# Performance work log

Measured on AMD Instinct MI355X. Metric: run time of the kernel, lower is better.

## Reference

```python
import jax, jax.numpy as jnp
import numpy as np

H = 2048          # hidden_size
I_MOE = 1408      # moe_intermediate_size (per expert)
I_SH = 5632       # shared_expert_intermediate_size
E = 8             # num_experts
TOP_K = 2         # num_experts_per_tok
B, S = 1, 2048


def setup_inputs() -> dict:
    key = jax.random.key(0)
    ks = jax.random.split(key, 7)
    sc = 0.02
    return {
        "hidden_states": jax.random.normal(ks[0], (B, S, H), jnp.float32),
        "W_router": jax.random.normal(ks[1], (E, H), jnp.float32) * sc,      # gate.weight
        "W_sgate": jax.random.normal(ks[2], (1, H), jnp.float32) * sc,       # shared_expert_gate.weight
        "Ws_gate_up": jax.random.normal(ks[3], (H, 2 * I_SH), jnp.float32) * sc,  # shared expert merged gate/up
        "Ws_down": jax.random.normal(ks[4], (I_SH, H), jnp.float32) * sc,
        "We_gate_up": jax.random.normal(ks[5], (E, H, 2 * I_MOE), jnp.float32) * sc,  # stacked expert gate/up
        "We_down": jax.random.normal(ks[6], (E, I_MOE, H), jnp.float32) * sc,
    }


def _silu_and_mul(gu, inter):
    # gate_up layout: [..., 2*inter] -> silu(gate) * up, matching SiluAndMul
    return jax.nn.silu(gu[..., :inter]) * gu[..., inter:]


def reference(hidden_states, W_router, W_sgate, Ws_gate_up, Ws_down, We_gate_up, We_down):
    orig_shape = hidden_states.shape
    x = hidden_states.reshape(-1, H)                     # [T, H]
    T = x.shape[0]

    # --- router: softmax in fp32 then top-k (NOT renormalized, as in source) ---
    logits = x @ W_router.T                              # [T, E]
    probs = jax.nn.softmax(logits.astype(jnp.float32), axis=-1)
    rw, sel = jax.lax.top_k(probs, TOP_K)                # [T, K]
    rw = rw.astype(x.dtype)

    # sparse combine matrix [T, E]: routing weight where selected, else 0
    combine = jnp.zeros((T, E), x.dtype).at[jnp.arange(T)[:, None], sel].add(rw)

    # --- shared expert ---
    sh = _silu_and_mul(x @ Ws_gate_up, I_SH) @ Ws_down    # [T, H]
    shared_out = sh * jax.nn.sigmoid(x @ W_sgate.T)       # [T, H]

    # --- experts: dense dispatch (math-identical to gather/MLP/index_add loop) ---
    gu = jnp.einsum('th,ehi->eti', x, We_gate_up)         # [E, T, 2*I_MOE]
    h = _silu_and_mul(gu, I_MOE)                          # [E, T, I_MOE]
    eo = jnp.einsum('eti,eih->eth', h, We_down)           # [E, T, H]
    sparse_out = jnp.einsum('eth,te->th', eo, combine)    # [T, H]

    return (shared_out + sparse_out).reshape(orig_shape)
```

## Files before the change

kernel.cpp:

```cpp
#include <hip/hip_runtime.h>
#include <cstdio>


#define H_DIM 2048
#define IMOE  1408
#define ISH   5632
#define NEXP  8
#define T_TOK 2048
#define TK_TOT (T_TOK * 2)

typedef __attribute__((ext_vector_type(8))) short short8;
typedef __attribute__((ext_vector_type(8))) __bf16 bf16x8;
typedef __attribute__((ext_vector_type(4))) float f32x4;

__device__ __forceinline__ float bf2f(unsigned short u) {
  union { unsigned int i; float f; } v; v.i = ((unsigned int)u) << 16; return v.f;
}
__device__ __forceinline__ unsigned short f2bf(float f) {
  union { float f; unsigned int i; } v; v.f = f;
  unsigned int x = v.i;
  return (unsigned short)((x + 0x7fffu + ((x >> 16) & 1u)) >> 16);
}

__device__ __forceinline__ f32x4 MFMA16(short8 a, short8 b, f32x4 c) {
  return __builtin_amdgcn_mfma_f32_16x16x32_bf16(
      __builtin_bit_cast(bf16x8, a), __builtin_bit_cast(bf16x8, b), c, 0, 0, 0);
}

__device__ __forceinline__ void gload_lds16(const unsigned short* g, unsigned short* l) {
  __builtin_amdgcn_global_load_lds(
      (const __attribute__((address_space(1))) unsigned int*)g,
      (__attribute__((address_space(3))) unsigned int*)l, 16, 0, 0);
}

__device__ __forceinline__ float silu_f(float x) { return x / (1.0f + __expf(-x)); }

#define SBAR()   asm volatile("s_barrier" ::: "memory")
#define VMCNT(n) asm volatile("s_waitcnt vmcnt(" #n ")" ::: "memory")


__global__ __launch_bounds__(256)
void transpose_cvt_kernel(const float* __restrict__ src, unsigned short* __restrict__ dst,
                          int R, int C, long sStride, long dStride) {
  src += (long)blockIdx.z * sStride;
  dst += (long)blockIdx.z * dStride;
  __shared__ float tile[32][33];
  int tx = threadIdx.x, ty = threadIdx.y;
  int x = blockIdx.x * 32 + tx;
  int yb = blockIdx.y * 32;
#pragma unroll
  for (int j = 0; j < 4; j++) {
    int y = yb + ty + j * 8;
    tile[ty + j * 8][tx] = src[(long)y * C + x];
  }
  __syncthreads();
  int c = blockIdx.x * 32 + ty;
  int r = yb + tx;
#pragma unroll
  for (int j = 0; j < 4; j++) {
    dst[(long)(c + j * 8) * R + r] = f2bf(tile[tx][ty + j * 8]);
  }
}

__global__ __launch_bounds__(256)
void cvt_x_kernel(const float* __restrict__ x, unsigned short* __restrict__ xb, int total4) {
  int i = blockIdx.x * 256 + threadIdx.x;
  if (i >= total4) return;
  float4 v = ((const float4*)x)[i];
  ushort4 o;
  o.x = f2bf(v.x); o.y = f2bf(v.y); o.z = f2bf(v.z); o.w = f2bf(v.w);
  ((ushort4*)xb)[i] = o;
}


__global__ __launch_bounds__(256)
void router_kernel(const float* __restrict__ x, const float* __restrict__ Wr,
                   const float* __restrict__ Wsg, float* __restrict__ rw,
                   int* __restrict__ sel, float* __restrict__ sgate_sig,
                   int* __restrict__ counts) {
  int t = blockIdx.x;
  const float* xr = x + (long)t * H_DIM;
  float p[9];
#pragma unroll
  for (int e = 0; e < 9; e++) p[e] = 0.0f;
  for (int h = threadIdx.x; h < H_DIM; h += 256) {
    float xv = xr[h];
#pragma unroll
    for (int e = 0; e < 8; e++) p[e] += xv * Wr[e * H_DIM + h];
    p[8] += xv * Wsg[h];
  }
#pragma unroll
  for (int e = 0; e < 9; e++)
    for (int off = 32; off > 0; off >>= 1)
      p[e] += __shfl_down(p[e], off, 64);
  __shared__ float red[4][9];
  int wave = threadIdx.x >> 6, lane = threadIdx.x & 63;
  if (lane == 0) {
#pragma unroll
    for (int e = 0; e < 9; e++) red[wave][e] = p[e];
  }
  __syncthreads();
  if (threadIdx.x == 0) {
    float lg[9];
#pragma unroll
    for (int e = 0; e < 9; e++) lg[e] = red[0][e] + red[1][e] + red[2][e] + red[3][e];
    float m = lg[0];
#pragma unroll
    for (int e = 1; e < 8; e++) m = fmaxf(m, lg[e]);
    float pr[8], s = 0.0f;
#pragma unroll
    for (int e = 0; e < 8; e++) { pr[e] = expf(lg[e] - m); s += pr[e]; }
    float inv = 1.0f / s;
#pragma unroll
    for (int e = 0; e < 8; e++) pr[e] *= inv;
    int i0 = 0;
#pragma unroll
    for (int e = 1; e < 8; e++) if (pr[e] > pr[i0]) i0 = e;
    int i1 = (i0 == 0) ? 1 : 0;
#pragma unroll
    for (int e = 0; e < 8; e++) if (e != i0 && pr[e] > pr[i1]) i1 = e;
    rw[t * 2] = pr[i0]; rw[t * 2 + 1] = pr[i1];
    sel[t * 2] = i0;    sel[t * 2 + 1] = i1;
    sgate_sig[t] = 1.0f / (1.0f + expf(-lg[8]));
    atomicAdd(&counts[i0], 1);
    atomicAdd(&counts[i1], 1);
  }
}

__global__ void scan_kernel(const int* __restrict__ counts, int* __restrict__ offsets) {
  if (threadIdx.x == 0 && blockIdx.x == 0) {
    int s = 0;
    for (int e = 0; e < NEXP; e++) { offsets[e] = s; s += counts[e]; }
    offsets[NEXP] = s;
  }
}

__global__ __launch_bounds__(256)
void scatter_kernel(const int* __restrict__ sel, const int* __restrict__ offsets,
                    int* __restrict__ cursor, int* __restrict__ tok_of_slot,
                    int* __restrict__ slot_of_tok) {
  int t = blockIdx.x * 256 + threadIdx.x;
  if (t >= T_TOK) return;
#pragma unroll
  for (int k = 0; k < 2; k++) {
    int e = sel[t * 2 + k];
    int pos = atomicAdd(&cursor[e], 1);
    int slot = offsets[e] + pos;
    tok_of_slot[slot] = t;
    slot_of_tok[t * 2 + k] = slot;
  }
}

template <int EPI, bool EXPERT, bool GATHER>
__global__ __launch_bounds__(512, 2)
void gemm8_kernel(const unsigned short* __restrict__ A,
                  const unsigned short* __restrict__ BT,
                  void* __restrict__ Cv,
                  int N, int Kld, int KLEN, int M,
                  const int* __restrict__ counts, const int* __restrict__ offsets,
                  const int* __restrict__ tok_of_slot,
                  const float* __restrict__ rowscale, long bt_estride) {
  __shared__ unsigned short lds8[65536];

  int cnt = M, rowbase = 0, k0 = 0;
  const unsigned short* bt = BT;
  if constexpr (EXPERT) {
    int e = blockIdx.z;
    cnt = counts[e];
    rowbase = offsets[e];
    bt += (long)e * bt_estride;
  } else {
    k0 = blockIdx.z * KLEN;
  }
  int row0 = blockIdx.x * 256;
  if (row0 >= cnt) return;
  int col0 = blockIdx.y * 256;

  int tid = threadIdx.x, wave = tid >> 6, lane = tid & 63;
  int NT = KLEN / 32;

  const unsigned short* aSrc[2];
  const unsigned short* bSrc[2];
#pragma unroll
  for (int i = 0; i < 2; i++) {
    int r = i * 128 + (tid >> 2);
    int sw = (((tid & 3) ^ ((r >> 1) & 3)) * 8);
    long arow;
    if constexpr (EXPERT) {
      int s = rowbase + min(row0 + r, cnt - 1);
      arow = GATHER ? tok_of_slot[s] : s;
    } else {
      arow = row0 + r;
    }
    aSrc[i] = A + arow * (long)Kld + k0 + sw;
    bSrc[i] = bt + (long)(col0 + r) * Kld + k0 + sw;
  }
  int dA0 = wave * 512, dA1 = 4096 + wave * 512;
  int dB0 = 8192 + wave * 512, dB1 = 12288 + wave * 512;

  auto STAGE_A = [&](int u) {
    int b2 = (u & 3) * 16384;
    long kk = (long)min(u, NT - 1) * 32;
    gload_lds16(aSrc[0] + kk, &lds8[b2 + dA0]);
    gload_lds16(aSrc[1] + kk, &lds8[b2 + dA1]);
  };
  auto STAGE_B = [&](int u) {
    int b2 = (u & 3) * 16384;
    long kk = (long)min(u, NT - 1) * 32;
    gload_lds16(bSrc[0] + kk, &lds8[b2 + dB0]);
    gload_lds16(bSrc[1] + kk, &lds8[b2 + dB1]);
  };

  int wr = wave >> 2, wc = wave & 3;
  int fr = lane & 15, fg = lane >> 4;
  int addrA0[4], addrA1[4], addrB[4];
#pragma unroll
  for (int m = 0; m < 4; m++) {
    int rl0 = wr * 128 + m * 16 + fr;
    int rl1 = rl0 + 64;
    int cl  = wc * 64 + m * 16 + fr;
    addrA0[m] = rl0 * 32 + ((fg ^ ((rl0 >> 1) & 3)) * 8);
    addrA1[m] = rl1 * 32 + ((fg ^ ((rl1 >> 1) & 3)) * 8);
    addrB[m]  = 8192 + cl * 32 + ((fg ^ ((cl >> 1) & 3)) * 8);
  }

  STAGE_A(0); STAGE_B(0);
  STAGE_A(1); STAGE_B(1);
  STAGE_A(2); STAGE_B(2);
  VMCNT(8);
  SBAR();

  f32x4 acc[8][4] = {};

  for (int t = 0; t < NT; t++) {
    int b = (t & 3) * 16384;
    int u = t + 3;
    short8 Bf[4], Af[4];
#pragma unroll
    for (int n = 0; n < 4; n++) Bf[n] = *(const short8*)&lds8[b + addrB[n]];
#pragma unroll
    for (int m = 0; m < 4; m++) Af[m] = *(const short8*)&lds8[b + addrA0[m]];
    STAGE_A(u);
    SBAR();
    __builtin_amdgcn_s_setprio(1);
#pragma unroll
    for (int m = 0; m < 4; m++)
#pragma unroll
      for (int n = 0; n < 4; n++)
        acc[m][n] = MFMA16(Af[m], Bf[n], acc[m][n]);
    __builtin_amdgcn_s_setprio(0);
    SBAR();
#pragma unroll
    for (int m = 0; m < 4; m++) Af[m] = *(const short8*)&lds8[b + addrA1[m]];
    STAGE_B(u);
    SBAR();
    __builtin_amdgcn_s_setprio(1);
#pragma unroll
    for (int m = 0; m < 4; m++)
#pragma unroll
      for (int n = 0; n < 4; n++)
        acc[4 + m][n] = MFMA16(Af[m], Bf[n], acc[4 + m][n]);
    __builtin_amdgcn_s_setprio(0);
    VMCNT(8);
    SBAR();
  }
  VMCNT(0);

  int rowguard = cnt - row0;
#pragma unroll
  for (int mq = 0; mq < 8; mq++) {
    int rl = wr * 128 + (mq >> 2) * 64 + (mq & 3) * 16 + fg * 4;
#pragma unroll
    for (int n = 0; n < 4; n++) {
      int cg = col0 + wc * 64 + n * 16 + fr;
      f32x4 v = acc[mq][n];
#pragma unroll
      for (int j = 0; j < 4; j++) {
        int r = rl + j;
        if (r < rowguard) {
          long orow = (long)rowbase + row0 + r;
          long ci = orow * (long)N + cg;
          if constexpr (EPI == 0)      ((unsigned short*)Cv)[ci] = f2bf(v[j]);
          else if constexpr (EPI == 2) ((float*)Cv)[ci] = v[j];
          else unsafeAtomicAdd(&((float*)Cv)[ci], v[j] * rowscale[orow]);
        }
      }
    }
  }
}


__global__ __launch_bounds__(256)
void silu_mul_kernel(const unsigned short* __restrict__ gu, unsigned short* __restrict__ h,
                     int rows, int I) {
  int i = blockIdx.x * 256 + threadIdx.x;
  int i4 = I >> 2;
  if (i >= rows * i4) return;
  int row = i / i4;
  int ci = (i - row * i4) * 4;
  const unsigned short* g = gu + (long)row * 2 * I + ci;
  ushort4 gv = *(const ushort4*)g;
  ushort4 uv = *(const ushort4*)(g + I);
  ushort4 o;
  o.x = f2bf(silu_f(bf2f(gv.x)) * bf2f(uv.x));
  o.y = f2bf(silu_f(bf2f(gv.y)) * bf2f(uv.y));
  o.z = f2bf(silu_f(bf2f(gv.z)) * bf2f(uv.z));
  o.w = f2bf(silu_f(bf2f(gv.w)) * bf2f(uv.w));
  *(ushort4*)(h + (long)row * I + ci) = o;
}

__global__ __launch_bounds__(256)
void combine_kernel(float* __restrict__ out, const float* __restrict__ eo,
                    const int* __restrict__ slot_of_tok, const float* __restrict__ rw) {
  int i = blockIdx.x * 256 + threadIdx.x;
  const int h4n = H_DIM / 4;
  if (i >= T_TOK * h4n) return;
  int t = i / h4n;
  int h4 = i - t * h4n;
  int s0 = slot_of_tok[t * 2], s1 = slot_of_tok[t * 2 + 1];
  float w0 = rw[t * 2], w1 = rw[t * 2 + 1];
  float4 o = ((float4*)out)[i];
  float4 a = ((const float4*)eo)[(long)s0 * h4n + h4];
  float4 b = ((const float4*)eo)[(long)s1 * h4n + h4];
  o.x += w0 * a.x + w1 * b.x;
  o.y += w0 * a.y + w1 * b.y;
  o.z += w0 * a.z + w1 * b.z;
  o.w += w0 * a.w + w1 * b.w;
  ((float4*)out)[i] = o;
}


extern "C" void kernel_launch(void* const* d_in, const int* in_sizes, int n_in,
                              void* d_out, int out_size, void* d_ws, size_t ws_size,
                              hipStream_t stream) {
  (void)in_sizes; (void)n_in; (void)out_size;
  const float* x    = (const float*)d_in[0];
  const float* Wr   = (const float*)d_in[1];
  const float* Wsg  = (const float*)d_in[2];
  const float* Wsgu = (const float*)d_in[3];
  const float* Wsd  = (const float*)d_in[4];
  const float* Wegu = (const float*)d_in[5];
  const float* Wed  = (const float*)d_in[6];
  float* out = (float*)d_out;

  char* ws = (char*)d_ws;
  size_t off = 0;
  auto alloc = [&](size_t b) { size_t o = off; off += (b + 255) & ~(size_t)255; return o; };

  size_t o_xbf   = alloc((size_t)T_TOK * H_DIM * 2);
  size_t o_WsguT = alloc((size_t)2 * ISH * H_DIM * 2);
  size_t o_WsdT  = alloc((size_t)H_DIM * ISH * 2);
  size_t o_WeguT = alloc((size_t)NEXP * 2 * IMOE * H_DIM * 2);
  size_t o_WedT  = alloc((size_t)NEXP * H_DIM * IMOE * 2);
  size_t o_gush  = alloc((size_t)T_TOK * 2 * ISH * 2);
  size_t o_hsh   = alloc((size_t)T_TOK * ISH * 2);
  size_t o_ints  = alloc(256);
  size_t o_rw    = alloc((size_t)TK_TOT * 4);
  size_t o_sel   = alloc((size_t)TK_TOT * 4);
  size_t o_sg    = alloc((size_t)T_TOK * 4);
  size_t o_tok   = alloc((size_t)TK_TOT * 4);
  size_t o_s2t   = alloc((size_t)TK_TOT * 4);

  if (off > ws_size) {
    fprintf(stderr, "[moe kernel] workspace too small: need %zu have %zu\n", off, ws_size);
    return;
  }

  unsigned short* xbf   = (unsigned short*)(ws + o_xbf);
  unsigned short* WsguT = (unsigned short*)(ws + o_WsguT);
  unsigned short* WsdT  = (unsigned short*)(ws + o_WsdT);
  unsigned short* WeguT = (unsigned short*)(ws + o_WeguT);
  unsigned short* WedT  = (unsigned short*)(ws + o_WedT);
  unsigned short* gu_sh = (unsigned short*)(ws + o_gush);
  unsigned short* h_sh  = (unsigned short*)(ws + o_hsh);
  unsigned short* gu_e = (unsigned short*)(ws + o_gush);
  unsigned short* h_e  = (unsigned short*)(ws + o_gush + (size_t)TK_TOT * 2 * IMOE * 2);
  float* eo = (float*)(ws + o_WsguT);

  int* counts  = (int*)(ws + o_ints);
  int* cursor  = counts + 8;
  int* offsets = counts + 16;
  float* rw    = (float*)(ws + o_rw);
  int* sel     = (int*)(ws + o_sel);
  float* sgate = (float*)(ws + o_sg);
  int* tok     = (int*)(ws + o_tok);
  int* s2t     = (int*)(ws + o_s2t);

  dim3 tb(32, 8, 1);

  hipMemsetAsync(counts, 0, 64, stream);

  transpose_cvt_kernel<<<dim3(2 * ISH / 32, H_DIM / 32, 1), tb, 0, stream>>>(
      Wsgu, WsguT, H_DIM, 2 * ISH, 0, 0);
  transpose_cvt_kernel<<<dim3(H_DIM / 32, ISH / 32, 1), tb, 0, stream>>>(
      Wsd, WsdT, ISH, H_DIM, 0, 0);
  transpose_cvt_kernel<<<dim3(2 * IMOE / 32, H_DIM / 32, NEXP), tb, 0, stream>>>(
      Wegu, WeguT, H_DIM, 2 * IMOE, (long)H_DIM * 2 * IMOE, (long)2 * IMOE * H_DIM);
  transpose_cvt_kernel<<<dim3(H_DIM / 32, IMOE / 32, NEXP), tb, 0, stream>>>(
      Wed, WedT, IMOE, H_DIM, (long)IMOE * H_DIM, (long)H_DIM * IMOE);

  cvt_x_kernel<<<(T_TOK * H_DIM / 4) / 256, 256, 0, stream>>>(x, xbf, T_TOK * H_DIM / 4);

  router_kernel<<<T_TOK, 256, 0, stream>>>(x, Wr, Wsg, rw, sel, sgate, counts);
  scan_kernel<<<1, 64, 0, stream>>>(counts, offsets);
  scatter_kernel<<<(T_TOK + 255) / 256, 256, 0, stream>>>(sel, offsets, cursor, tok, s2t);

  gemm8_kernel<0, false, false><<<dim3(T_TOK / 256, 2 * ISH / 256, 1), 512, 0, stream>>>(
      xbf, WsguT, gu_sh, 2 * ISH, H_DIM, H_DIM, T_TOK,
      nullptr, nullptr, nullptr, nullptr, 0);
  silu_mul_kernel<<<(T_TOK * (ISH / 4)) / 256, 256, 0, stream>>>(gu_sh, h_sh, T_TOK, ISH);

  hipMemsetAsync(out, 0, (size_t)T_TOK * H_DIM * 4, stream);
  gemm8_kernel<1, false, false><<<dim3(T_TOK / 256, H_DIM / 256, 4), 512, 0, stream>>>(
      h_sh, WsdT, out, H_DIM, ISH, ISH / 4, T_TOK,
      nullptr, nullptr, nullptr, sgate, 0);

  gemm8_kernel<0, true, true><<<dim3(T_TOK / 256, 2 * IMOE / 256, NEXP), 512, 0, stream>>>(
      xbf, WeguT, gu_e, 2 * IMOE, H_DIM, H_DIM, 0,
      counts, offsets, tok, nullptr, (long)2 * IMOE * H_DIM);
  silu_mul_kernel<<<(TK_TOT * (IMOE / 4)) / 256, 256, 0, stream>>>(gu_e, h_e, TK_TOT, IMOE);
  gemm8_kernel<2, true, false><<<dim3(T_TOK / 256, H_DIM / 256, NEXP), 512, 0, stream>>>(
      h_e, WedT, eo, H_DIM, IMOE, IMOE, 0,
      counts, offsets, nullptr, nullptr, (long)H_DIM * IMOE);

  combine_kernel<<<(T_TOK * H_DIM / 4) / 256, 256, 0, stream>>>(out, eo, s2t, rw);
}
```

Baseline: 760.3 us.

## Fuse SiLU-and-mul into gate/up GEMM epilogue via interleaved weights; pre-gather expert tokens

The transpose of the gate/up weights now interleaves gate and up columns, so each adjacent pair of output columns in the GEMM holds a gate and its matching up value. The epilogue uses a lane shuffle to pair them, applies SiLU-times-up, and writes the half-width bf16 activation directly. This removes the separate silu_mul kernels and the full-width gate/up intermediate round trip to memory. A gather kernel copies the routed tokens into a contiguous buffer, so the expert GEMM no longer does indirect row loads; this adds one extra copy pass over 4096x2048 bf16.

```diff
diff --git a/kernel.cpp b/kernel.cpp
--- a/kernel.cpp
+++ b/kernel.cpp
@@ -39,9 +39,10 @@
 #define VMCNT(n) asm volatile("s_waitcnt vmcnt(" #n ")" ::: "memory")
 
 
+template <bool ILV>
 __global__ __launch_bounds__(256)
 void transpose_cvt_kernel(const float* __restrict__ src, unsigned short* __restrict__ dst,
-                          int R, int C, long sStride, long dStride) {
+                          int R, int C, int I, long sStride, long dStride) {
   src += (long)blockIdx.z * sStride;
   dst += (long)blockIdx.z * dStride;
   __shared__ float tile[32][33];
@@ -54,11 +55,12 @@
     tile[ty + j * 8][tx] = src[(long)y * C + x];
   }
   __syncthreads();
-  int c = blockIdx.x * 32 + ty;
   int r = yb + tx;
 #pragma unroll
   for (int j = 0; j < 4; j++) {
-    dst[(long)(c + j * 8) * R + r] = f2bf(tile[tx][ty + j * 8]);
+    int c = blockIdx.x * 32 + ty + j * 8;
+    int cd = ILV ? (c < I ? 2 * c : 2 * (c - I) + 1) : c;
+    dst[(long)cd * R + r] = f2bf(tile[tx][ty + j * 8]);
   }
 }
 
@@ -149,6 +151,16 @@
     tok_of_slot[slot] = t;
     slot_of_tok[t * 2 + k] = slot;
   }
+}
+
+__global__ __launch_bounds__(256)
+void gather_kernel(const unsigned short* __restrict__ xbf, const int* __restrict__ tok,
+                   unsigned short* __restrict__ xg) {
+  int i = blockIdx.x * 256 + threadIdx.x;
+  int slot = i >> 8, c8 = i & 255;
+  long src = (long)tok[slot] * H_DIM + c8 * 8;
+  ulonglong2 v = *(const ulonglong2*)(xbf + src);
+  ((ulonglong2*)xg)[i] = v;
 }
 
 template <int EPI, bool EXPERT, bool GATHER>
@@ -277,37 +289,25 @@
 #pragma unroll
       for (int j = 0; j < 4; j++) {
         int r = rl + j;
+        float pv = __shfl_xor(v[j], 1);
         if (r < rowguard) {
           long orow = (long)rowbase + row0 + r;
-          long ci = orow * (long)N + cg;
-          if constexpr (EPI == 0)      ((unsigned short*)Cv)[ci] = f2bf(v[j]);
-          else if constexpr (EPI == 2) ((float*)Cv)[ci] = v[j];
-          else unsafeAtomicAdd(&((float*)Cv)[ci], v[j] * rowscale[orow]);
+          if constexpr (EPI == 1) {
+            unsafeAtomicAdd(&((float*)Cv)[orow * (long)N + cg], v[j] * rowscale[orow]);
+          } else if constexpr (EPI == 2) {
+            ((float*)Cv)[orow * (long)N + cg] = v[j];
+          } else {
+            if (!(fr & 1)) {
+              float hval = silu_f(v[j]) * pv;
+              ((unsigned short*)Cv)[orow * (long)(N >> 1) + (cg >> 1)] = f2bf(hval);
+            }
+          }
         }
       }
     }
   }
 }
 
-
-__global__ __launch_bounds__(256)
-void silu_mul_kernel(const unsigned short* __restrict__ gu, unsigned short* __restrict__ h,
-                     int rows, int I) {
-  int i = blockIdx.x * 256 + threadIdx.x;
-  int i4 = I >> 2;
-  if (i >= rows * i4) return;
-  int row = i / i4;
-  int ci = (i - row * i4) * 4;
-  const unsigned short* g = gu + (long)row * 2 * I + ci;
-  ushort4 gv = *(const ushort4*)g;
-  ushort4 uv = *(const ushort4*)(g + I);
-  ushort4 o;
-  o.x = f2bf(silu_f(bf2f(gv.x)) * bf2f(uv.x));
-  o.y = f2bf(silu_f(bf2f(gv.y)) * bf2f(uv.y));
-  o.z = f2bf(silu_f(bf2f(gv.z)) * bf2f(uv.z));
-  o.w = f2bf(silu_f(bf2f(gv.w)) * bf2f(uv.w));
-  *(ushort4*)(h + (long)row * I + ci) = o;
-}
 
 __global__ __launch_bounds__(256)
 void combine_kernel(float* __restrict__ out, const float* __restrict__ eo,
@@ -352,8 +352,9 @@
   size_t o_WsdT  = alloc((size_t)H_DIM * ISH * 2);
   size_t o_WeguT = alloc((size_t)NEXP * 2 * IMOE * H_DIM * 2);
   size_t o_WedT  = alloc((size_t)NEXP * H_DIM * IMOE * 2);
-  size_t o_gush  = alloc((size_t)T_TOK * 2 * ISH * 2);
   size_t o_hsh   = alloc((size_t)T_TOK * ISH * 2);
+  size_t o_he    = alloc((size_t)TK_TOT * IMOE * 2);
+  size_t o_xg    = alloc((size_t)TK_TOT * H_DIM * 2);
   size_t o_ints  = alloc(256);
   size_t o_rw    = alloc((size_t)TK_TOT * 4);
   size_t o_sel   = alloc((size_t)TK_TOT * 4);
@@ -371,15 +372,15 @@
   unsigned short* WsdT  = (unsigned short*)(ws + o_WsdT);
   unsigned short* WeguT = (unsigned short*)(ws + o_WeguT);
   unsigned short* WedT  = (unsigned short*)(ws + o_WedT);
-  unsigned short* gu_sh = (unsigned short*)(ws + o_gush);
   unsigned short* h_sh  = (unsigned short*)(ws + o_hsh);
-  unsigned short* gu_e = (unsigned short*)(ws + o_gush);
-  unsigned short* h_e  = (unsigned short*)(ws + o_gush + (size_t)TK_TOT * 2 * IMOE * 2);
-  float* eo = (float*)(ws + o_WsguT);
-
-  int* counts  = (int*)(ws + o_ints);
-  int* cursor  = counts + 8;
-  int* offsets = counts + 16;
+  unsigned short* h_e   = (unsigned short*)(ws + o_he);
+  unsigned short* xg    = (unsigned short*)(ws + o_xg);
+  float* eo             = (float*)(ws + o_WsguT);
+
+  int* ints    = (int*)(ws + o_ints);
+  int* counts  = ints;
+  int* cursor  = ints + 8;
+  int* offsets = ints + 16;
   float* rw    = (float*)(ws + o_rw);
   int* sel     = (int*)(ws + o_sel);
   float* sgate = (float*)(ws + o_sg);
@@ -388,37 +389,37 @@
 
   dim3 tb(32, 8, 1);
 
-  hipMemsetAsync(counts, 0, 64, stream);
-
-  transpose_cvt_kernel<<<dim3(2 * ISH / 32, H_DIM / 32, 1), tb, 0, stream>>>(
-      Wsgu, WsguT, H_DIM, 2 * ISH, 0, 0);
-  transpose_cvt_kernel<<<dim3(H_DIM / 32, ISH / 32, 1), tb, 0, stream>>>(
-      Wsd, WsdT, ISH, H_DIM, 0, 0);
-  transpose_cvt_kernel<<<dim3(2 * IMOE / 32, H_DIM / 32, NEXP), tb, 0, stream>>>(
-      Wegu, WeguT, H_DIM, 2 * IMOE, (long)H_DIM * 2 * IMOE, (long)2 * IMOE * H_DIM);
-  transpose_cvt_kernel<<<dim3(H_DIM / 32, IMOE / 32, NEXP), tb, 0, stream>>>(
-      Wed, WedT, IMOE, H_DIM, (long)IMOE * H_DIM, (long)H_DIM * IMOE);
+  hipMemsetAsync(ints, 0, 64, stream);
+  hipMemsetAsync(out, 0, (size_t)T_TOK * H_DIM * 4, stream);
+
+  transpose_cvt_kernel<true><<<dim3(2 * ISH / 32, H_DIM / 32, 1), tb, 0, stream>>>(
+      Wsgu, WsguT, H_DIM, 2 * ISH, ISH, 0, 0);
+  transpose_cvt_kernel<false><<<dim3(H_DIM / 32, ISH / 32, 1), tb, 0, stream>>>(
+      Wsd, WsdT, ISH, H_DIM, 0, 0, 0);
+  transpose_cvt_kernel<true><<<dim3(2 * IMOE / 32, H_DIM / 32, NEXP), tb, 0, stream>>>(
+      Wegu, WeguT, H_DIM, 2 * IMOE, IMOE, (long)H_DIM * 2 * IMOE, (long)2 * IMOE * H_DIM);
+  transpose_cvt_kernel<false><<<dim3(H_DIM / 32, IMOE / 32, NEXP), tb, 0, stream>>>(
+      Wed, WedT, IMOE, H_DIM, 0, (long)IMOE * H_DIM, (long)H_DIM * IMOE);
 
   cvt_x_kernel<<<(T_TOK * H_DIM / 4) / 256, 256, 0, stream>>>(x, xbf, T_TOK * H_DIM / 4);
 
   router_kernel<<<T_TOK, 256, 0, stream>>>(x, Wr, Wsg, rw, sel, sgate, counts);
   scan_kernel<<<1, 64, 0, stream>>>(counts, offsets);
   scatter_kernel<<<(T_TOK + 255) / 256, 256, 0, stream>>>(sel, offsets, cursor, tok, s2t);
-
-  gemm8_kernel<0, false, false><<<dim3(T_TOK / 256, 2 * ISH / 256, 1), 512, 0, stream>>>(
-      xbf, WsguT, gu_sh, 2 * ISH, H_DIM, H_DIM, T_TOK,
+  gather_kernel<<<TK_TOT, 256, 0, stream>>>(xbf, tok, xg);
+
+  gemm8_kernel<3, false, false><<<dim3(T_TOK / 256, 2 * ISH / 256, 1), 512, 0, stream>>>(
+      xbf, WsguT, h_sh, 2 * ISH, H_DIM, H_DIM, T_TOK,
       nullptr, nullptr, nullptr, nullptr, 0);
-  silu_mul_kernel<<<(T_TOK * (ISH / 4)) / 256, 256, 0, stream>>>(gu_sh, h_sh, T_TOK, ISH);
-
-  hipMemsetAsync(out, 0, (size_t)T_TOK * H_DIM * 4, stream);
+
+  gemm8_kernel<3, true, false><<<dim3(T_TOK / 256, 2 * IMOE / 256, NEXP), 512, 0, stream>>>(
+      xg, WeguT, h_e, 2 * IMOE, H_DIM, H_DIM, 0,
+      counts, offsets, nullptr, nullptr, (long)2 * IMOE * H_DIM);
+
   gemm8_kernel<1, false, false><<<dim3(T_TOK / 256, H_DIM / 256, 4), 512, 0, stream>>>(
       h_sh, WsdT, out, H_DIM, ISH, ISH / 4, T_TOK,
       nullptr, nullptr, nullptr, sgate, 0);
 
-  gemm8_kernel<0, true, true><<<dim3(T_TOK / 256, 2 * IMOE / 256, NEXP), 512, 0, stream>>>(
-      xbf, WeguT, gu_e, 2 * IMOE, H_DIM, H_DIM, 0,
-      counts, offsets, tok, nullptr, (long)2 * IMOE * H_DIM);
-  silu_mul_kernel<<<(TK_TOT * (IMOE / 4)) / 256, 256, 0, stream>>>(gu_e, h_e, TK_TOT, IMOE);
   gemm8_kernel<2, true, false><<<dim3(T_TOK / 256, H_DIM / 256, NEXP), 512, 0, stream>>>(
       h_e, WedT, eo, H_DIM, IMOE, IMOE, 0,
       counts, offsets, nullptr, nullptr, (long)H_DIM * IMOE);
```

New measurement: 797.5 us. 1.05x slower.
